# Kernel tuning notes

Hardware: AMD Instinct MI355X
Metric: run time of the kernel (lower is better)

## Reference

```python
import jax, jax.numpy as jnp
import numpy as np

N, F, H, C, E = 100000, 512, 128, 8, 1600000
GAMMA = 1.0
EPS = 1e-8


def _xavier(key, shape):
    a = np.sqrt(6.0 / (shape[0] + shape[1])).astype(np.float32)
    return jax.random.uniform(key, shape, jnp.float32, -a, a)


def _agg(w, x, src, dst):
    # y[i] = sum_{e: dst[e]==i} w[e] * x[src[e]]  (sparse adj @ x)
    return jax.ops.segment_sum(w[:, None] * x[src], dst, num_segments=N)


def setup_inputs() -> dict:
    key = jax.random.key(0)
    ks = jax.random.split(key, 8)
    features = jax.random.normal(ks[0], (N, F), jnp.float32)
    edge_src = jax.random.randint(ks[1], (E,), 0, N)
    edge_dst = jax.random.randint(ks[2], (E,), 0, N)
    # degree-based normalized edge weights, mimicking D^p A D^p
    deg = jnp.zeros((N,), jnp.float32).at[edge_dst].add(1.0)
    deg = jnp.maximum(deg, 1.0)
    d_half = deg ** -0.5
    d_one = deg ** -1.0
    w1 = d_half[edge_dst] * d_half[edge_src]   # D^-1/2 A D^-1/2
    w2 = d_one[edge_dst] * d_one[edge_src]     # D^-1  A D^-1
    Wm1 = _xavier(ks[3], (F, H))
    Ws1 = _xavier(ks[4], (F, H))
    Wm2 = _xavier(ks[5], (H, C))
    Ws2 = _xavier(ks[6], (H, C))
    noise = jax.random.normal(ks[7], (N, C), jnp.float32)
    return {"features": features, "edge_src": edge_src, "edge_dst": edge_dst,
            "w1": w1, "w2": w2, "Wm1": Wm1, "Ws1": Ws1, "Wm2": Wm2,
            "Ws2": Ws2, "noise": noise}


def reference(features, edge_src, edge_dst, w1, w2, Wm1, Ws1, Wm2, Ws2, noise):
    # GGCL_F (eval mode: dropout is identity)
    miu1 = jax.nn.elu(features @ Wm1)
    sigma1 = jax.nn.relu(features @ Ws1)
    att1 = jnp.exp(-GAMMA * sigma1)
    miu_h = _agg(w1, miu1 * att1, edge_src, edge_dst)
    sigma_h = _agg(w2, sigma1 * att1 * att1, edge_src, edge_dst)
    # GGCL_D
    miu2 = jax.nn.elu(miu_h @ Wm2)
    sigma2 = jax.nn.relu(sigma_h @ Ws2)
    att2 = jnp.exp(-GAMMA * sigma2)
    mean_out = _agg(w1, miu2 * att2, edge_src, edge_dst)
    # GGCL_D returns (mean_out, sigma2); reparameterized sample
    return mean_out + noise * jnp.sqrt(sigma2 + EPS)
```

## Files before the change

kernel.cpp:

```cpp
#include <hip/hip_runtime.h>
#include <cstdint>

#define AS1 __attribute__((address_space(1)))
#define AS3 __attribute__((address_space(3)))

typedef __attribute__((ext_vector_type(8))) short short8;
typedef __attribute__((ext_vector_type(4))) float floatx4;
typedef unsigned short u16;

static constexpr int NN   = 100000;
static constexpr int FF   = 512;
static constexpr int HH   = 128;
static constexpr int EE   = 1600000;
static constexpr int PADM = 100096;
static constexpr int NPAD = 100352;
static constexpr int NB   = 98;

__device__ __forceinline__ u16 f2bf_rne(float v) {
    uint32_t u = __builtin_bit_cast(uint32_t, v);
    u += 0x7fffu + ((u >> 16) & 1u);
    return (u16)(u >> 16);
}
__device__ __forceinline__ float bf2f(u16 h) {
    uint32_t u = ((uint32_t)h) << 16;
    return __builtin_bit_cast(float, u);
}
__device__ __forceinline__ void async16(const void* g, void* l) {
    __builtin_amdgcn_global_load_lds((AS1 const void*)g, (AS3 void*)l, 16, 0, 0);
}

__global__ void k_split_w(const float* __restrict__ Wm1, const float* __restrict__ Ws1,
                          u16* __restrict__ whi, u16* __restrict__ wlo) {
    int t = blockIdx.x * 256 + threadIdx.x;
    int n = t >> 9, k = t & 511;
    float v = (n < HH) ? Wm1[k * HH + n] : Ws1[k * HH + (n - HH)];
    u16 h = f2bf_rne(v);
    whi[t] = h;
    wlo[t] = f2bf_rne(v - bf2f(h));
}

__global__ void k_prep_w2(const float* __restrict__ Wm2, const float* __restrict__ Ws2,
                          u16* __restrict__ W2B) {
    int t = blockIdx.x * 256 + threadIdx.x;
    int j = t & 7, l = (t >> 3) & 63, kc = (t >> 9) & 3, p = t >> 11;
    int n = l & 15, quad = l >> 4;
    int k = kc * 32 + quad * 8 + j;
    float v = 0.f;
    if (n < 8) {
        float wv = (p == 0) ? Wm2[k * 8 + n] : Ws2[k * 8 + n];
        v = (p == 2) ? (wv - bf2f(f2bf_rne(wv))) : wv;
    }
    W2B[t] = f2bf_rne(v);
}

__global__ void k_deg(const int* __restrict__ dst, int* __restrict__ deg) {
    int e = blockIdx.x * 256 + threadIdx.x;
    atomicAdd(&deg[dst[e]], 1);
}
__global__ void k_dh(const int* __restrict__ deg, float2* __restrict__ dd) {
    int t = blockIdx.x * 256 + threadIdx.x;
    int d = max(deg[t], 1);
    float df = (float)d;
    dd[t] = make_float2(1.f / sqrtf(df), 1.f / df);
}

__global__ __launch_bounds__(512, 4) void k_gemm(
        const float* __restrict__ A,
        const u16* __restrict__ BhiG, const u16* __restrict__ BloG,
        const u16* __restrict__ W2B, const float2* __restrict__ dd,
        float* __restrict__ Z) {
    __shared__ u16 sm[20480];
    const int tid = threadIdx.x;
    const int w = tid >> 6, lane = tid & 63;
    const int ml = lane & 15, quad = lane >> 4;
    const int wrow = w & 1, wcol = w >> 1;
    const int rowBase = blockIdx.x * 128;

    floatx4 am[4][2], as_[4][2];
#pragma unroll
    for (int i = 0; i < 4; i++)
#pragma unroll
        for (int j = 0; j < 2; j++) {
            am[i][j]  = (floatx4){0.f, 0.f, 0.f, 0.f};
            as_[i][j] = (floatx4){0.f, 0.f, 0.f, 0.f};
        }

    const int r0 = tid >> 2, q0 = tid & 3;
    const int key0 = (r0 >> 1) & 3;
    const int ko  = q0 * 8;
    const int kob = (q0 ^ key0) * 8;
    const int arow = min(rowBase + r0, NN - 1);
    const float* gA = A + (size_t)arow * FF + ko;
    const u16* gBh = BhiG + (size_t)r0 * FF + kob;
    const u16* gBl = BloG + (size_t)(128 + r0) * FF + kob;

    const int awr = r0 * 32 + (q0 ^ key0) * 8;

    const int xq = (ml >> 1) & 3;
    const int aoff = (wrow * 64 + ml) * 32 + (quad ^ xq) * 8;
    const int bmo  = 8192  + (32 * wcol + ml) * 32 + (quad ^ xq) * 8;
    const int bso  = 12288 + (32 * wcol + ml) * 32 + (quad ^ xq) * 8;
    const int blo_ = 16384 + (32 * wcol + ml) * 32 + (quad ^ xq) * 8;

    for (int kt = 0; kt < FF; kt += 32) {
        __syncthreads();
        async16(gBh + kt,                      &sm[8192  + tid * 8]);
        async16(gBh + (size_t)128 * FF + kt,   &sm[12288 + tid * 8]);
        async16(gBl + kt,                      &sm[16384 + tid * 8]);
        {
            const float4* pA = (const float4*)(gA + kt);
            float4 x0 = pA[0], x1 = pA[1];
            float xv[8] = {x0.x, x0.y, x0.z, x0.w, x1.x, x1.y, x1.z, x1.w};
            short8 hv, lv;
#pragma unroll
            for (int q = 0; q < 8; q++) {
                u16 hh = f2bf_rne(xv[q]);
                hv[q] = (short)hh;
                lv[q] = (short)f2bf_rne(xv[q] - bf2f(hh));
            }
            *(short8*)&sm[awr] = hv;
            *(short8*)&sm[4096 + awr] = lv;
        }
        __syncthreads();

        short8 ah[4], al[4];
#pragma unroll
        for (int i = 0; i < 4; i++) ah[i] = *(const short8*)&sm[aoff + i * 512];
#pragma unroll
        for (int i = 0; i < 4; i++) al[i] = *(const short8*)&sm[4096 + aoff + i * 512];
#pragma unroll
        for (int jm = 0; jm < 2; jm++) {
            short8 b = *(const short8*)&sm[bmo + jm * 512];
#pragma unroll
            for (int i = 0; i < 4; i++)
                am[i][jm] = __builtin_amdgcn_mfma_f32_16x16x32_bf16(ah[i], b, am[i][jm], 0, 0, 0);
        }
#pragma unroll
        for (int js = 0; js < 2; js++) {
            short8 bh = *(const short8*)&sm[bso + js * 512];
            short8 bl = *(const short8*)&sm[blo_ + js * 512];
#pragma unroll
            for (int i = 0; i < 4; i++) {
                floatx4 c = as_[i][js];
                c = __builtin_amdgcn_mfma_f32_16x16x32_bf16(ah[i], bh, c, 0, 0, 0);
                c = __builtin_amdgcn_mfma_f32_16x16x32_bf16(ah[i], bl, c, 0, 0, 0);
                c = __builtin_amdgcn_mfma_f32_16x16x32_bf16(al[i], bh, c, 0, 0, 0);
                as_[i][js] = c;
            }
        }
    }

    short8 wm[4], wsh[4], wsl[4];
#pragma unroll
    for (int kc = 0; kc < 4; kc++) {
        wm[kc]  = *(const short8*)&W2B[(kc * 64 + lane) * 8];
        wsh[kc] = *(const short8*)&W2B[2048 + (kc * 64 + lane) * 8];
        wsl[kc] = *(const short8*)&W2B[4096 + (kc * 64 + lane) * 8];
    }
    const int rg = w & 1, pp = w >> 1;

#pragma unroll
    for (int h = 0; h < 4; h++) {
        __syncthreads();
        if (wrow == (h >> 1)) {
#pragma unroll
            for (int ii = 0; ii < 2; ii++) {
                int i = (h & 1) * 2 + ii;
#pragma unroll
                for (int jm = 0; jm < 2; jm++) {
                    int c = 32 * wcol + 16 * jm + ml;
#pragma unroll
                    for (int r = 0; r < 4; r++) {
                        int lr = ii * 16 + quad * 4 + r;
                        float2 d2 = dd[rowBase + h * 32 + lr];
                        float u = am[i][jm][r], v = as_[i][jm][r];
                        float m1 = u > 0.f ? u : __expf(u) - 1.f;
                        float s1 = v > 0.f ? v : 0.f;
                        float a1 = __expf(-s1);
                        float xmv = d2.x * m1 * a1;
                        float xsv = d2.y * s1 * a1 * a1;
                        u16 hh = f2bf_rne(xsv);
                        sm[lr * 136 + c]        = f2bf_rne(xmv);
                        sm[4352 + lr * 136 + c] = hh;
                        sm[8704 + lr * 136 + c] = f2bf_rne(xsv - bf2f(hh));
                    }
                }
            }
        }
        __syncthreads();
        if (w < 4) {
            floatx4 z = (floatx4){0.f, 0.f, 0.f, 0.f};
#pragma unroll
            for (int kc = 0; kc < 4; kc++) {
                if (pp == 0) {
                    short8 a = *(const short8*)&sm[(rg * 16 + ml) * 136 + kc * 32 + quad * 8];
                    z = __builtin_amdgcn_mfma_f32_16x16x32_bf16(a, wm[kc], z, 0, 0, 0);
                } else {
                    short8 a = *(const short8*)&sm[4352 + (rg * 16 + ml) * 136 + kc * 32 + quad * 8];
                    short8 b = *(const short8*)&sm[8704 + (rg * 16 + ml) * 136 + kc * 32 + quad * 8];
                    z = __builtin_amdgcn_mfma_f32_16x16x32_bf16(a, wsh[kc], z, 0, 0, 0);
                    z = __builtin_amdgcn_mfma_f32_16x16x32_bf16(a, wsl[kc], z, 0, 0, 0);
                    z = __builtin_amdgcn_mfma_f32_16x16x32_bf16(b, wsh[kc], z, 0, 0, 0);
                }
            }
            if (ml < 8) {
                int rowb = rowBase + h * 32 + rg * 16 + quad * 4;
#pragma unroll
                for (int r = 0; r < 4; r++)
                    if (rowb + r < NN) Z[(size_t)(rowb + r) * 16 + pp * 8 + ml] = z[r];
            }
        }
    }
}

__global__ void k_scan1(const int* __restrict__ deg, int* __restrict__ bsum) {
    int t = threadIdx.x;
    int4 v = ((const int4*)deg)[blockIdx.x * 256 + t];
    __shared__ int red[256];
    red[t] = v.x + v.y + v.z + v.w;
    __syncthreads();
    for (int o = 128; o > 0; o >>= 1) {
        if (t < o) red[t] += red[t + o];
        __syncthreads();
    }
    if (t == 0) bsum[blockIdx.x] = red[0];
}

__global__ void k_scan2(const int* __restrict__ bsum, int* __restrict__ boff) {
    int t = threadIdx.x;
    __shared__ int s[128];
    int own = (t < NB) ? bsum[t] : 0;
    s[t] = own;
    __syncthreads();
    for (int o = 1; o < 128; o <<= 1) {
        int v = (t >= o) ? s[t - o] : 0;
        __syncthreads();
        s[t] += v;
        __syncthreads();
    }
    if (t < NB) boff[t] = s[t] - own;
}

__global__ void k_scan3(const int* __restrict__ deg, const int* __restrict__ boff,
                        int* __restrict__ ptr, int* __restrict__ cursor) {
    int t = threadIdx.x;
    int gi = blockIdx.x * 256 + t;
    int4 v = ((const int4*)deg)[gi];
    int tsum = v.x + v.y + v.z + v.w;
    __shared__ int s[256];
    s[t] = tsum;
    __syncthreads();
    for (int o = 1; o < 256; o <<= 1) {
        int pv = (t >= o) ? s[t - o] : 0;
        __syncthreads();
        s[t] += pv;
        __syncthreads();
    }
    int base = boff[blockIdx.x] + (s[t] - tsum);
    int4 e;
    e.x = base;
    e.y = base + v.x;
    e.z = e.y + v.y;
    e.w = e.z + v.z;
    ((int4*)ptr)[gi] = e;
    ((int4*)cursor)[gi] = e;
}

__global__ void k_scatter(const int* __restrict__ src, const int* __restrict__ dst,
                          int* __restrict__ cursor, int* __restrict__ pay) {
    int e = blockIdx.x * 256 + threadIdx.x;
    int d = dst[e];
    int p = atomicAdd(&cursor[d], 1);
    int pr = pay[p];
    asm volatile("" :: "v"(pr) : "memory");
    pay[p] = src[e];
}

__global__ __launch_bounds__(256) void k_aggA(const int* __restrict__ ptr,
        const int* __restrict__ pay, const float* __restrict__ Z,
        const float2* __restrict__ dd, const float* __restrict__ noise,
        float* __restrict__ y, float* __restrict__ out) {
    int wave = threadIdx.x >> 6, lane = threadIdx.x & 63;
    int i = blockIdx.x * 4 + wave;
    if (i >= NN) return;
    int er = lane >> 3, c = lane & 7;
    int s0 = ptr[i], e0 = ptr[i + 1];
    float am = 0.f, as_ = 0.f;
    int j = s0 + er;
    int sidx = (j < e0) ? pay[j] : -1;
    while (sidx >= 0) {
        int jn = j + 8;
        int snext = (jn < e0) ? pay[jn] : -1;
        const float* zr = Z + (size_t)sidx * 16;
        am  += zr[c];
        as_ += zr[8 + c];
        j = jn;
        sidx = snext;
    }
    am  += __shfl_xor(am, 8, 64);
    am  += __shfl_xor(am, 16, 64);
    am  += __shfl_xor(am, 32, 64);
    as_ += __shfl_xor(as_, 8, 64);
    as_ += __shfl_xor(as_, 16, 64);
    as_ += __shfl_xor(as_, 32, 64);
    if (lane < 8) {
        float2 d2 = dd[i];
        float hm = d2.x * am, hs = d2.y * as_;
        float miu2 = hm > 0.f ? hm : __expf(hm) - 1.f;
        float s2 = hs > 0.f ? hs : 0.f;
        y[i * 8 + lane]   = d2.x * miu2 * __expf(-s2);
        out[i * 8 + lane] = noise[i * 8 + lane] * sqrtf(s2 + 1e-8f);
    }
}

__global__ __launch_bounds__(256) void k_aggB(const int* __restrict__ ptr,
        const int* __restrict__ pay, const float* __restrict__ y,
        const float2* __restrict__ dd, float* __restrict__ out) {
    int wave = threadIdx.x >> 6, lane = threadIdx.x & 63;
    int i = blockIdx.x * 4 + wave;
    if (i >= NN) return;
    int er = lane >> 3, c = lane & 7;
    int s0 = ptr[i], e0 = ptr[i + 1];
    float acc = 0.f;
    int j = s0 + er;
    int sidx = (j < e0) ? pay[j] : -1;
    while (sidx >= 0) {
        int jn = j + 8;
        int snext = (jn < e0) ? pay[jn] : -1;
        acc += y[(size_t)sidx * 8 + c];
        j = jn;
        sidx = snext;
    }
    acc += __shfl_xor(acc, 8, 64);
    acc += __shfl_xor(acc, 16, 64);
    acc += __shfl_xor(acc, 32, 64);
    if (lane < 8) out[i * 8 + lane] += dd[i].x * acc;
}

extern "C" void kernel_launch(void* const* d_in, const int* in_sizes, int n_in,
                              void* d_out, int out_size, void* d_ws, size_t ws_size,
                              hipStream_t stream) {
    (void)in_sizes; (void)n_in; (void)out_size; (void)ws_size;
    const float* feat  = (const float*)d_in[0];
    const int*   esrc  = (const int*)d_in[1];
    const int*   edst  = (const int*)d_in[2];
    const float* Wm1   = (const float*)d_in[5];
    const float* Ws1   = (const float*)d_in[6];
    const float* Wm2   = (const float*)d_in[7];
    const float* Ws2   = (const float*)d_in[8];
    const float* noise = (const float*)d_in[9];
    float* out = (float*)d_out;

    char* ws = (char*)d_ws;
    size_t off = 0;
    auto alloc = [&](size_t bytes) -> void* {
        void* p = ws + off;
        off += (bytes + 255) & ~(size_t)255;
        return p;
    };
    u16*    WhiT = (u16*)alloc((size_t)256 * 512 * 2);
    u16*    WloT = (u16*)alloc((size_t)256 * 512 * 2);
    u16*    W2B  = (u16*)alloc((size_t)6144 * 2);
    float*  Z    = (float*)alloc((size_t)NN * 16 * 4);
    float*  yb   = (float*)alloc((size_t)NN * 8 * 4);
    int*    deg  = (int*)alloc((size_t)NPAD * 4);
    float2* dd   = (float2*)alloc((size_t)NPAD * 8);
    int*    ptr  = (int*)alloc((size_t)(NPAD + 4) * 4);
    int*    cur  = (int*)alloc((size_t)NPAD * 4);
    int*    bsum = (int*)alloc(256 * 4);
    int*    boff = (int*)alloc(256 * 4);
    int*    pay  = (int*)alloc((size_t)EE * 4);

    hipMemsetAsync(deg, 0, (size_t)NPAD * 4, stream);

    k_deg    <<<EE / 256, 256, 0, stream>>>(edst, deg);
    k_dh     <<<NPAD / 256, 256, 0, stream>>>(deg, dd);
    k_scan1  <<<NB, 256, 0, stream>>>(deg, bsum);
    k_scan2  <<<1, 128, 0, stream>>>(bsum, boff);
    k_scan3  <<<NB, 256, 0, stream>>>(deg, boff, ptr, cur);
    k_scatter<<<EE / 256, 256, 0, stream>>>(esrc, edst, cur, pay);

    k_split_w<<<512, 256, 0, stream>>>(Wm1, Ws1, WhiT, WloT);
    k_prep_w2<<<24, 256, 0, stream>>>(Wm2, Ws2, W2B);
    k_gemm   <<<PADM / 128, 512, 0, stream>>>(feat, WhiT, WloT, W2B, dd, Z);

    k_aggA<<<(NN + 3) / 4, 256, 0, stream>>>(ptr, pay, Z, dd, noise, yb, out);
    k_aggB<<<(NN + 3) / 4, 256, 0, stream>>>(ptr, pay, yb, dd, out);
}
```

Measured before the change: 607.2 us.

## Shrink GEMM row tile to 32 rows with 256-thread blocks

Changes the fused feature GEMM from 128-row tiles with 512 threads to 32-row tiles with 256 threads. Each wave now covers one 32-column slice of all 32 rows, and the epilogue runs in a single pass instead of four. This gives about four times as many blocks (around 3128 versus 782) and less LDS per block, so occupancy and load balance across CUs should improve. In exchange, the weight tiles are reloaded per 32 rows rather than per 128, which cuts weight reuse and increases L2 traffic for the B operand.

```diff
diff --git a/kernel.cpp b/kernel.cpp
--- a/kernel.cpp
+++ b/kernel.cpp
@@ -64,21 +64,21 @@
     dd[t] = make_float2(1.f / sqrtf(df), 1.f / df);
 }
 
-__global__ __launch_bounds__(512, 4) void k_gemm(
+__global__ __launch_bounds__(256, 5) void k_gemm(
         const float* __restrict__ A,
         const u16* __restrict__ BhiG, const u16* __restrict__ BloG,
         const u16* __restrict__ W2B, const float2* __restrict__ dd,
         float* __restrict__ Z) {
-    __shared__ u16 sm[20480];
+    __shared__ u16 sm[14336];
     const int tid = threadIdx.x;
     const int w = tid >> 6, lane = tid & 63;
     const int ml = lane & 15, quad = lane >> 4;
-    const int wrow = w & 1, wcol = w >> 1;
-    const int rowBase = blockIdx.x * 128;
-
-    floatx4 am[4][2], as_[4][2];
-#pragma unroll
-    for (int i = 0; i < 4; i++)
+    const int wcol = w;
+    const int rowBase = blockIdx.x * 32;
+
+    floatx4 am[2][2], as_[2][2];
+#pragma unroll
+    for (int i = 0; i < 2; i++)
 #pragma unroll
         for (int j = 0; j < 2; j++) {
             am[i][j]  = (floatx4){0.f, 0.f, 0.f, 0.f};
@@ -87,27 +87,32 @@
 
     const int r0 = tid >> 2, q0 = tid & 3;
     const int key0 = (r0 >> 1) & 3;
-    const int ko  = q0 * 8;
     const int kob = (q0 ^ key0) * 8;
-    const int arow = min(rowBase + r0, NN - 1);
-    const float* gA = A + (size_t)arow * FF + ko;
     const u16* gBh = BhiG + (size_t)r0 * FF + kob;
     const u16* gBl = BloG + (size_t)(128 + r0) * FF + kob;
 
-    const int awr = r0 * 32 + (q0 ^ key0) * 8;
+    const int ar = tid >> 2, aq = tid & 3;
+    const int akey = (ar >> 1) & 3;
+    const int arow = min(rowBase + ar, NN - 1);
+    const float* gA = A + (size_t)arow * FF + aq * 8;
+    const int awr = ar * 32 + (aq ^ akey) * 8;
 
     const int xq = (ml >> 1) & 3;
-    const int aoff = (wrow * 64 + ml) * 32 + (quad ^ xq) * 8;
-    const int bmo  = 8192  + (32 * wcol + ml) * 32 + (quad ^ xq) * 8;
-    const int bso  = 12288 + (32 * wcol + ml) * 32 + (quad ^ xq) * 8;
-    const int blo_ = 16384 + (32 * wcol + ml) * 32 + (quad ^ xq) * 8;
+    const int qx = (quad ^ xq) * 8;
+    const int aoff = ml * 32 + qx;
+    const int bmo  = 2048  + (32 * wcol + ml) * 32 + qx;
+    const int bso  = 6144  + (32 * wcol + ml) * 32 + qx;
+    const int blo_ = 10240 + (32 * wcol + ml) * 32 + qx;
 
     for (int kt = 0; kt < FF; kt += 32) {
         __syncthreads();
-        async16(gBh + kt,                      &sm[8192  + tid * 8]);
-        async16(gBh + (size_t)128 * FF + kt,   &sm[12288 + tid * 8]);
-        async16(gBl + kt,                      &sm[16384 + tid * 8]);
-        {
+        async16(gBh + kt,                      &sm[2048  + tid * 8]);
+        async16(gBh + (size_t)64  * FF + kt,   &sm[4096  + tid * 8]);
+        async16(gBh + (size_t)128 * FF + kt,   &sm[6144  + tid * 8]);
+        async16(gBh + (size_t)192 * FF + kt,   &sm[8192  + tid * 8]);
+        async16(gBl + kt,                      &sm[10240 + tid * 8]);
+        async16(gBl + (size_t)64  * FF + kt,   &sm[12288 + tid * 8]);
+        if (tid < 128) {
             const float4* pA = (const float4*)(gA + kt);
             float4 x0 = pA[0], x1 = pA[1];
             float xv[8] = {x0.x, x0.y, x0.z, x0.w, x1.x, x1.y, x1.z, x1.w};
@@ -119,20 +124,20 @@
                 lv[q] = (short)f2bf_rne(xv[q] - bf2f(hh));
             }
             *(short8*)&sm[awr] = hv;
-            *(short8*)&sm[4096 + awr] = lv;
-        }
-        __syncthreads();
-
-        short8 ah[4], al[4];
-#pragma unroll
-        for (int i = 0; i < 4; i++) ah[i] = *(const short8*)&sm[aoff + i * 512];
-#pragma unroll
-        for (int i = 0; i < 4; i++) al[i] = *(const short8*)&sm[4096 + aoff + i * 512];
+            *(short8*)&sm[1024 + awr] = lv;
+        }
+        __syncthreads();
+
+        short8 ah[2], al[2];
+#pragma unroll
+        for (int i = 0; i < 2; i++) ah[i] = *(const short8*)&sm[aoff + i * 512];
+#pragma unroll
+        for (int i = 0; i < 2; i++) al[i] = *(const short8*)&sm[1024 + aoff + i * 512];
 #pragma unroll
         for (int jm = 0; jm < 2; jm++) {
             short8 b = *(const short8*)&sm[bmo + jm * 512];
 #pragma unroll
-            for (int i = 0; i < 4; i++)
+            for (int i = 0; i < 2; i++)
                 am[i][jm] = __builtin_amdgcn_mfma_f32_16x16x32_bf16(ah[i], b, am[i][jm], 0, 0, 0);
         }
 #pragma unroll
@@ -140,7 +145,7 @@
             short8 bh = *(const short8*)&sm[bso + js * 512];
             short8 bl = *(const short8*)&sm[blo_ + js * 512];
 #pragma unroll
-            for (int i = 0; i < 4; i++) {
+            for (int i = 0; i < 2; i++) {
                 floatx4 c = as_[i][js];
                 c = __builtin_amdgcn_mfma_f32_16x16x32_bf16(ah[i], bh, c, 0, 0, 0);
                 c = __builtin_amdgcn_mfma_f32_16x16x32_bf16(ah[i], bl, c, 0, 0, 0);
@@ -159,56 +164,50 @@
     }
     const int rg = w & 1, pp = w >> 1;
 
-#pragma unroll
-    for (int h = 0; h < 4; h++) {
-        __syncthreads();
-        if (wrow == (h >> 1)) {
-#pragma unroll
-            for (int ii = 0; ii < 2; ii++) {
-                int i = (h & 1) * 2 + ii;
-#pragma unroll
-                for (int jm = 0; jm < 2; jm++) {
-                    int c = 32 * wcol + 16 * jm + ml;
-#pragma unroll
-                    for (int r = 0; r < 4; r++) {
-                        int lr = ii * 16 + quad * 4 + r;
-                        float2 d2 = dd[rowBase + h * 32 + lr];
-                        float u = am[i][jm][r], v = as_[i][jm][r];
-                        float m1 = u > 0.f ? u : __expf(u) - 1.f;
-                        float s1 = v > 0.f ? v : 0.f;
-                        float a1 = __expf(-s1);
-                        float xmv = d2.x * m1 * a1;
-                        float xsv = d2.y * s1 * a1 * a1;
-                        u16 hh = f2bf_rne(xsv);
-                        sm[lr * 136 + c]        = f2bf_rne(xmv);
-                        sm[4352 + lr * 136 + c] = hh;
-                        sm[8704 + lr * 136 + c] = f2bf_rne(xsv - bf2f(hh));
-                    }
-                }
+    __syncthreads();
+#pragma unroll
+    for (int i = 0; i < 2; i++) {
+#pragma unroll
+        for (int jm = 0; jm < 2; jm++) {
+            int c = 32 * wcol + 16 * jm + ml;
+#pragma unroll
+            for (int r = 0; r < 4; r++) {
+                int lr = i * 16 + quad * 4 + r;
+                float2 d2 = dd[rowBase + lr];
+                float u = am[i][jm][r], v = as_[i][jm][r];
+                float m1 = u > 0.f ? u : __expf(u) - 1.f;
+                float s1 = v > 0.f ? v : 0.f;
+                float a1 = __expf(-s1);
+                float xmv = d2.x * m1 * a1;
+                float xsv = d2.y * s1 * a1 * a1;
+                u16 hh = f2bf_rne(xsv);
+                sm[lr * 136 + c]        = f2bf_rne(xmv);
+                sm[4352 + lr * 136 + c] = hh;
+                sm[8704 + lr * 136 + c] = f2bf_rne(xsv - bf2f(hh));
             }
         }
-        __syncthreads();
-        if (w < 4) {
-            floatx4 z = (floatx4){0.f, 0.f, 0.f, 0.f};
-#pragma unroll
-            for (int kc = 0; kc < 4; kc++) {
-                if (pp == 0) {
-                    short8 a = *(const short8*)&sm[(rg * 16 + ml) * 136 + kc * 32 + quad * 8];
-                    z = __builtin_amdgcn_mfma_f32_16x16x32_bf16(a, wm[kc], z, 0, 0, 0);
-                } else {
-                    short8 a = *(const short8*)&sm[4352 + (rg * 16 + ml) * 136 + kc * 32 + quad * 8];
-                    short8 b = *(const short8*)&sm[8704 + (rg * 16 + ml) * 136 + kc * 32 + quad * 8];
-                    z = __builtin_amdgcn_mfma_f32_16x16x32_bf16(a, wsh[kc], z, 0, 0, 0);
-                    z = __builtin_amdgcn_mfma_f32_16x16x32_bf16(a, wsl[kc], z, 0, 0, 0);
-                    z = __builtin_amdgcn_mfma_f32_16x16x32_bf16(b, wsh[kc], z, 0, 0, 0);
-                }
+    }
+    __syncthreads();
+    {
+        floatx4 z = (floatx4){0.f, 0.f, 0.f, 0.f};
+#pragma unroll
+        for (int kc = 0; kc < 4; kc++) {
+            if (pp == 0) {
+                short8 a = *(const short8*)&sm[(rg * 16 + ml) * 136 + kc * 32 + quad * 8];
+                z = __builtin_amdgcn_mfma_f32_16x16x32_bf16(a, wm[kc], z, 0, 0, 0);
+            } else {
+                short8 a = *(const short8*)&sm[4352 + (rg * 16 + ml) * 136 + kc * 32 + quad * 8];
+                short8 b = *(const short8*)&sm[8704 + (rg * 16 + ml) * 136 + kc * 32 + quad * 8];
+                z = __builtin_amdgcn_mfma_f32_16x16x32_bf16(a, wsh[kc], z, 0, 0, 0);
+                z = __builtin_amdgcn_mfma_f32_16x16x32_bf16(a, wsl[kc], z, 0, 0, 0);
+                z = __builtin_amdgcn_mfma_f32_16x16x32_bf16(b, wsh[kc], z, 0, 0, 0);
             }
-            if (ml < 8) {
-                int rowb = rowBase + h * 32 + rg * 16 + quad * 4;
-#pragma unroll
-                for (int r = 0; r < 4; r++)
-                    if (rowb + r < NN) Z[(size_t)(rowb + r) * 16 + pp * 8 + ml] = z[r];
-            }
+        }
+        if (ml < 8) {
+            int rowb = rowBase + rg * 16 + quad * 4;
+#pragma unroll
+            for (int r = 0; r < 4; r++)
+                if (rowb + r < NN) Z[(size_t)(rowb + r) * 16 + pp * 8 + ml] = z[r];
         }
     }
 }
@@ -382,7 +381,7 @@
 
     k_split_w<<<512, 256, 0, stream>>>(Wm1, Ws1, WhiT, WloT);
     k_prep_w2<<<24, 256, 0, stream>>>(Wm2, Ws2, W2B);
-    k_gemm   <<<PADM / 128, 512, 0, stream>>>(feat, WhiT, WloT, W2B, dd, Z);
+    k_gemm   <<<PADM / 32, 256, 0, stream>>>(feat, WhiT, WloT, W2B, dd, Z);
 
     k_aggA<<<(NN + 3) / 4, 256, 0, stream>>>(ptr, pay, Z, dd, noise, yb, out);
     k_aggB<<<(NN + 3) / 4, 256, 0, stream>>>(ptr, pay, yb, dd, out);
```

New measurement: 632.5 us. +4.2%, slower.

## Double-buffer GEMM k-loop with async fp32 A loads and in-register bf16 split

Applied to the files above, without the earlier changes.

The first GEMM's k-loop now double-buffers shared memory. The next tile of both A and B is fetched asynchronously while the current tile is computed, so each step needs one barrier instead of two. A is loaded raw as fp32 into LDS through a swizzled async copy, and each wave converts it to hi/lo bf16 in registers just before the MFMAs. This removes the separate convert-and-store phase and its synchronisation. The costs are double the shared memory, which may reduce occupancy, and a hi/lo split that now uses round-half-up with a truncated low part instead of RNE, which changes numerics slightly.

```diff
diff --git a/kernel.cpp b/kernel.cpp
--- a/kernel.cpp
+++ b/kernel.cpp
@@ -69,7 +69,7 @@
         const u16* __restrict__ BhiG, const u16* __restrict__ BloG,
         const u16* __restrict__ W2B, const float2* __restrict__ dd,
         float* __restrict__ Z) {
-    __shared__ u16 sm[20480];
+    __shared__ u16 sm[40960];
     const int tid = threadIdx.x;
     const int w = tid >> 6, lane = tid & 63;
     const int ml = lane & 15, quad = lane >> 4;
@@ -85,69 +85,83 @@
             as_[i][j] = (floatx4){0.f, 0.f, 0.f, 0.f};
         }
 
+    const int strow = tid >> 3;
+    const int g = (tid & 7) ^ (strow & 7);
+    const int arow1 = min(rowBase + strow, NN - 1);
+    const int arow2 = min(rowBase + 64 + strow, NN - 1);
+    const float* gA1 = A + (size_t)arow1 * FF + g * 4;
+    const float* gA2 = A + (size_t)arow2 * FF + g * 4;
+
     const int r0 = tid >> 2, q0 = tid & 3;
     const int key0 = (r0 >> 1) & 3;
-    const int ko  = q0 * 8;
     const int kob = (q0 ^ key0) * 8;
-    const int arow = min(rowBase + r0, NN - 1);
-    const float* gA = A + (size_t)arow * FF + ko;
     const u16* gBh = BhiG + (size_t)r0 * FF + kob;
     const u16* gBl = BloG + (size_t)(128 + r0) * FF + kob;
 
-    const int awr = r0 * 32 + (q0 ^ key0) * 8;
-
     const int xq = (ml >> 1) & 3;
-    const int aoff = (wrow * 64 + ml) * 32 + (quad ^ xq) * 8;
     const int bmo  = 8192  + (32 * wcol + ml) * 32 + (quad ^ xq) * 8;
     const int bso  = 12288 + (32 * wcol + ml) * 32 + (quad ^ xq) * 8;
     const int blo_ = 16384 + (32 * wcol + ml) * 32 + (quad ^ xq) * 8;
-
-    for (int kt = 0; kt < FF; kt += 32) {
-        __syncthreads();
-        async16(gBh + kt,                      &sm[8192  + tid * 8]);
-        async16(gBh + (size_t)128 * FF + kt,   &sm[12288 + tid * 8]);
-        async16(gBl + kt,                      &sm[16384 + tid * 8]);
-        {
-            const float4* pA = (const float4*)(gA + kt);
-            float4 x0 = pA[0], x1 = pA[1];
-            float xv[8] = {x0.x, x0.y, x0.z, x0.w, x1.x, x1.y, x1.z, x1.w};
-            short8 hv, lv;
+    const int akey = ml & 7;
+
+    auto stage = [&](int bb, int kt) {
+        async16(gA1 + kt, &sm[bb + tid * 8]);
+        async16(gA2 + kt, &sm[bb + 4096 + tid * 8]);
+        async16(gBh + kt,                      &sm[bb + 8192  + tid * 8]);
+        async16(gBh + (size_t)128 * FF + kt,   &sm[bb + 12288 + tid * 8]);
+        async16(gBl + kt,                      &sm[bb + 16384 + tid * 8]);
+    };
+
+    auto compute = [&](int cb) {
+        short8 bm[2], bh[2], bl[2];
+#pragma unroll
+        for (int jj = 0; jj < 2; jj++) {
+            bm[jj] = *(const short8*)&sm[cb + bmo  + jj * 512];
+            bh[jj] = *(const short8*)&sm[cb + bso  + jj * 512];
+            bl[jj] = *(const short8*)&sm[cb + blo_ + jj * 512];
+        }
+        const float4* af = (const float4*)&sm[cb];
+#pragma unroll
+        for (int i = 0; i < 4; i++) {
+            int row = wrow * 64 + i * 16 + ml;
+            float4 f0 = af[row * 8 + ((quad * 2 + 0) ^ akey)];
+            float4 f1 = af[row * 8 + ((quad * 2 + 1) ^ akey)];
+            float xv[8] = {f0.x, f0.y, f0.z, f0.w, f1.x, f1.y, f1.z, f1.w};
+            short8 ah, al;
 #pragma unroll
             for (int q = 0; q < 8; q++) {
-                u16 hh = f2bf_rne(xv[q]);
-                hv[q] = (short)hh;
-                lv[q] = (short)f2bf_rne(xv[q] - bf2f(hh));
+                uint32_t u = __builtin_bit_cast(uint32_t, xv[q]);
+                uint32_t uh = (u + 0x8000u) & 0xffff0000u;
+                ah[q] = (short)(uh >> 16);
+                float lof = xv[q] - __builtin_bit_cast(float, uh);
+                al[q] = (short)(__builtin_bit_cast(uint32_t, lof) >> 16);
             }
-            *(short8*)&sm[awr] = hv;
-            *(short8*)&sm[4096 + awr] = lv;
-        }
-        __syncthreads();
-
-        short8 ah[4], al[4];
-#pragma unroll
-        for (int i = 0; i < 4; i++) ah[i] = *(const short8*)&sm[aoff + i * 512];
-#pragma unroll
-        for (int i = 0; i < 4; i++) al[i] = *(const short8*)&sm[4096 + aoff + i * 512];
-#pragma unroll
-        for (int jm = 0; jm < 2; jm++) {
-            short8 b = *(const short8*)&sm[bmo + jm * 512];
-#pragma unroll
-            for (int i = 0; i < 4; i++)
-                am[i][jm] = __builtin_amdgcn_mfma_f32_16x16x32_bf16(ah[i], b, am[i][jm], 0, 0, 0);
-        }
-#pragma unroll
-        for (int js = 0; js < 2; js++) {
-            short8 bh = *(const short8*)&sm[bso + js * 512];
-            short8 bl = *(const short8*)&sm[blo_ + js * 512];
-#pragma unroll
-            for (int i = 0; i < 4; i++) {
+            am[i][0] = __builtin_amdgcn_mfma_f32_16x16x32_bf16(ah, bm[0], am[i][0], 0, 0, 0);
+            am[i][1] = __builtin_amdgcn_mfma_f32_16x16x32_bf16(ah, bm[1], am[i][1], 0, 0, 0);
+#pragma unroll
+            for (int js = 0; js < 2; js++) {
                 floatx4 c = as_[i][js];
-                c = __builtin_amdgcn_mfma_f32_16x16x32_bf16(ah[i], bh, c, 0, 0, 0);
-                c = __builtin_amdgcn_mfma_f32_16x16x32_bf16(ah[i], bl, c, 0, 0, 0);
-                c = __builtin_amdgcn_mfma_f32_16x16x32_bf16(al[i], bh, c, 0, 0, 0);
+                c = __builtin_amdgcn_mfma_f32_16x16x32_bf16(ah, bh[js], c, 0, 0, 0);
+                c = __builtin_amdgcn_mfma_f32_16x16x32_bf16(ah, bl[js], c, 0, 0, 0);
+                c = __builtin_amdgcn_mfma_f32_16x16x32_bf16(al, bh[js], c, 0, 0, 0);
                 as_[i][js] = c;
             }
         }
+    };
+
+    stage(0, 0);
+    asm volatile("s_waitcnt vmcnt(0)" ::: "memory");
+    __builtin_amdgcn_s_barrier();
+    asm volatile("" ::: "memory");
+
+    int cur = 0;
+    for (int kt = 0; kt < FF; kt += 32) {
+        if (kt + 32 < FF) stage((cur ^ 1) * 20480, kt + 32);
+        compute(cur * 20480);
+        asm volatile("s_waitcnt vmcnt(0) lgkmcnt(0)" ::: "memory");
+        __builtin_amdgcn_s_barrier();
+        asm volatile("" ::: "memory");
+        cur ^= 1;
     }
 
     short8 wm[4], wsh[4], wsl[4];
```

New measurement: 612.5 us. About the same (+0.9%).
